# Performance work log

Measured on AMD Instinct MI355X. Metric: run time of the kernel, lower is better.

Reference implementation:

```python
import jax, jax.numpy as jnp
import numpy as np

MARGIN = 1.0
EPS = 1e-6  # torch.nn.PairwiseDistance default eps (added to the difference vector)


def setup_inputs() -> dict:
    key = jax.random.key(0)
    k1, k2 = jax.random.split(key)
    B, D = 8192, 256
    out = jax.random.normal(k1, (B, D), dtype=jnp.float32)
    label = jax.random.randint(k2, (B,), 0, 2, dtype=jnp.int64)
    return {"out": out, "label": label}


def reference(out, label):
    B, D = out.shape
    # PairwiseDistance: dist_ij = || out_i - out_j + eps ||_2
    # Expand: sum_k (d_k + eps)^2 = ||d||^2 + 2*eps*sum_k d_k + D*eps^2
    sq_norm = jnp.sum(out * out, axis=-1)                       # [B]
    gram = out @ out.T                                          # [B, B]
    sq = sq_norm[:, None] + sq_norm[None, :] - 2.0 * gram       # ||out_i - out_j||^2
    row_sum = jnp.sum(out, axis=-1)                             # [B]
    sq_eps = sq + 2.0 * EPS * (row_sum[:, None] - row_sum[None, :]) + D * EPS * EPS
    dist = jnp.sqrt(jnp.maximum(sq_eps, 1e-12))                 # [B, B]

    same = label[:, None] == label[None, :]                     # [B, B] bool
    pos = dist * dist
    neg = jnp.square(jnp.maximum(MARGIN - dist, 0.0))
    per_pair = jnp.where(same, pos, neg)

    # only i < j pairs (strict upper triangle)
    tri = jnp.triu(jnp.ones((B, B), dtype=out.dtype), k=1)
    loss = jnp.sum(per_pair * tri)
    cnt = B * (B - 1) // 2
    return loss / (cnt + 1e-6)
```

## Files before the change

### kernel.cpp

```cpp
#include <hip/hip_runtime.h>
#include <hip/hip_bf16.h>
#include <hip/hip_fp8.h>

#define B_ 8192
#define D_ 256
#define EPS_ 1e-6f
#define MARGIN_ 1.0f
#define NT_ 64
#define NTILES_ (NT_ * (NT_ + 1) / 2)
#define CEPS_ ((float)D_ * EPS_ * EPS_)

typedef float floatx4 __attribute__((ext_vector_type(4)));

typedef __attribute__((address_space(3))) unsigned int lds_uint_t;
typedef __attribute__((address_space(1))) const unsigned int g_uint_t;

__device__ __forceinline__ void g2l16(const unsigned char* g, unsigned char* l) {
    __builtin_amdgcn_global_load_lds((g_uint_t*)g, (lds_uint_t*)l, 16, 0, 0);
}

#define XBF_BYTES (B_ * D_ * 2)
#define OFF_P      0
#define OFF_Q      8192
#define OFF_TP0    16384
#define OFF_TP1    81920
#define OFF_PPP    147456
#define OFF_QQP    147968
#define OFF_CP     148480
#define OFF_PMINP  148736
#define OFF_QMINP  148992
#define OFF_ACC    149248

__device__ __forceinline__ int trif(int t) { return (t * (129 - t)) / 2; }
__device__ __forceinline__ int decode_ti(int t) {
    int ti = (int)((129.0f - sqrtf(fmaxf(16641.0f - 8.0f * (float)t, 0.0f))) * 0.5f);
    ti = max(0, min(63, ti));
    while (trif(ti + 1) <= t) ++ti;
    while (trif(ti) > t) --ti;
    return ti;
}

__global__ __launch_bounds__(256) void prep_kernel(
    const float* __restrict__ x, const int* __restrict__ label,
    unsigned char* __restrict__ xq, float* __restrict__ fws) {
    float* p = fws + OFF_P;   float* q = fws + OFF_Q;
    float* Tp0 = fws + OFF_TP0; float* Tp1 = fws + OFF_TP1;
    float* PpP = fws + OFF_PPP; float* QqP = fws + OFF_QQP;
    float* CpP = fws + OFF_CP;
    float* pminP = fws + OFF_PMINP; float* qminP = fws + OFF_QMINP;
    float* acc = fws + OFF_ACC;

    __shared__ int lab_s[32];
    __shared__ float spl[32], sql[32];
    __shared__ float colbuf0[4][256], colbuf1[4][256];

    const int blk = blockIdx.x;
    const int r0 = blk * 32;
    const int tid = threadIdx.x, w = tid >> 6, lane = tid & 63;

    if (tid < 32) lab_s[tid] = label[r0 + tid];
    __syncthreads();

    floatx4 t0 = (floatx4)0.0f, t1 = (floatx4)0.0f;
    #pragma unroll
    for (int i = 0; i < 8; ++i) {
        const int rloc = w * 8 + i;
        const int row = r0 + rloc;
        const floatx4 v = *(const floatx4*)(x + (size_t)row * D_ + lane * 4);
        float sq = v[0]*v[0] + v[1]*v[1] + v[2]*v[2] + v[3]*v[3];
        float rs = v[0] + v[1] + v[2] + v[3];
        #pragma unroll
        for (int off = 32; off; off >>= 1) {
            sq += __shfl_down(sq, off);
            rs += __shfl_down(rs, off);
        }
        if (lane == 0) {
            const float pv = sq + 2.0f * EPS_ * rs;
            const float qv = sq - 2.0f * EPS_ * rs;
            p[row] = pv; q[row] = qv; spl[rloc] = pv; sql[rloc] = qv;
        }
        if (lab_s[rloc]) t1 += v; else t0 += v;
        __hip_fp8_e4m3 c0(v[0]), c1(v[1]), c2(v[2]), c3(v[3]);
        const unsigned int u = (unsigned int)c0.__x | ((unsigned int)c1.__x << 8)
                             | ((unsigned int)c2.__x << 16) | ((unsigned int)c3.__x << 24);
        *(unsigned int*)(xq + (size_t)row * D_ + lane * 4) = u;
    }
    *(floatx4*)&colbuf0[w][lane * 4] = t0;
    *(floatx4*)&colbuf1[w][lane * 4] = t1;
    __syncthreads();

    {
        const int c = tid;
        Tp0[blk * 256 + c] = colbuf0[0][c] + colbuf0[1][c] + colbuf0[2][c] + colbuf0[3][c];
        Tp1[blk * 256 + c] = colbuf1[0][c] + colbuf1[1][c] + colbuf1[2][c] + colbuf1[3][c];
    }
    if (tid < 64) {
        const bool va = tid < 32;
        const float pv = va ? spl[tid & 31] : 0.0f;
        const float qv = va ? sql[tid & 31] : 0.0f;
        const int lb = va ? lab_s[tid & 31] : 0;
        float p0 = (va && !lb) ? pv : 0.0f, p1 = (va && lb) ? pv : 0.0f;
        float q0 = (va && !lb) ? qv : 0.0f, q1 = (va && lb) ? qv : 0.0f;
        float c0 = (va && !lb) ? 1.0f : 0.0f;
        float pm = va ? pv : 1e30f, qm = va ? qv : 1e30f;
        #pragma unroll
        for (int off = 32; off; off >>= 1) {
            p0 += __shfl_down(p0, off); p1 += __shfl_down(p1, off);
            q0 += __shfl_down(q0, off); q1 += __shfl_down(q1, off);
            c0 += __shfl_down(c0, off);
            pm = fminf(pm, __shfl_down(pm, off));
            qm = fminf(qm, __shfl_down(qm, off));
        }
        if (tid == 0) {
            PpP[blk * 2 + 0] = p0; PpP[blk * 2 + 1] = p1;
            QqP[blk * 2 + 0] = q0; QqP[blk * 2 + 1] = q1;
            CpP[blk] = c0; pminP[blk] = pm; qminP[blk] = qm;
            if (blk == 0) acc[0] = 0.0f;
        }
    }
}

__global__ __launch_bounds__(256, 2) void tile_kernel(
    const unsigned char* __restrict__ xq, const float* __restrict__ x,
    const int* __restrict__ label, const float* __restrict__ fws,
    float* __restrict__ acc) {
    const float* p = fws + OFF_P;  const float* q = fws + OFF_Q;
    const float* pminP = fws + OFF_PMINP; const float* qminP = fws + OFF_QMINP;

    const int ti = decode_ti(blockIdx.x);
    const int tj = ti + (blockIdx.x - trif(ti));
    const int i0 = ti * 128, j0 = tj * 128;

    __shared__ __align__(16) unsigned char As[128 * 256];
    __shared__ __align__(16) unsigned char Bs[128 * 256];

    const int tid = threadIdx.x, wave = tid >> 6, lane = tid & 63;
    const int quad = lane >> 4, r = lane & 15;
    const int wm = wave >> 1, wn = wave & 1;

    const int rL4 = lane >> 4, c16 = lane & 15;
    {
        const unsigned char* gA = xq + (size_t)(i0 + wave * 32) * D_;
        const unsigned char* gB = xq + (size_t)(j0 + wave * 32) * D_;
        #pragma unroll
        for (int i = 0; i < 8; ++i) {
            const int rr = i * 4 + rL4;
            const int key = rr & 7;
            const int srcoff = rr * 256 + ((c16 ^ key) * 16);
            g2l16(gA + srcoff, &As[(wave * 32 + i * 4) * 256]);
            g2l16(gB + srcoff, &Bs[(wave * 32 + i * 4) * 256]);
        }
    }

    int rbA[4], rbB[4];
    #pragma unroll
    for (int mt = 0; mt < 4; ++mt) rbA[mt] = (wm * 64 + mt * 16 + r) * 256;
    #pragma unroll
    for (int nt = 0; nt < 4; ++nt) rbB[nt] = (wn * 64 + nt * 16 + r) * 256;
    const int q8 = (quad & 1) * 8, qh = quad >> 1, r7 = r & 7;

    floatx4 accv[16];
    #pragma unroll
    for (int t = 0; t < 16; ++t) accv[t] = (floatx4)0.0f;

    __syncthreads();

    #pragma unroll
    for (int kb = 0; kb < 8; ++kb) {
        const int pcb = (((kb * 2 + qh) ^ r7) * 16) + q8;
        long av[4], bv[4];
        #pragma unroll
        for (int mt = 0; mt < 4; ++mt) av[mt] = *(const long*)(As + rbA[mt] + pcb);
        #pragma unroll
        for (int nt = 0; nt < 4; ++nt) bv[nt] = *(const long*)(Bs + rbB[nt] + pcb);
        #pragma unroll
        for (int mt = 0; mt < 4; ++mt)
            #pragma unroll
            for (int nt = 0; nt < 4; ++nt)
                accv[mt * 4 + nt] = __builtin_amdgcn_mfma_f32_16x16x32_fp8_fp8(
                    av[mt], bv[nt], accv[mt * 4 + nt], 0, 0, 0);
    }

    if (ti != tj) {
        float m = -1e30f;
        #pragma unroll
        for (int t = 0; t < 16; ++t)
            m = fmaxf(m, fmaxf(fmaxf(accv[t][0], accv[t][1]), fmaxf(accv[t][2], accv[t][3])));
        const float pmn = fminf(fminf(pminP[4 * ti], pminP[4 * ti + 1]),
                                fminf(pminP[4 * ti + 2], pminP[4 * ti + 3]));
        const float qmn = fminf(fminf(qminP[4 * tj], qminP[4 * tj + 1]),
                                fminf(qminP[4 * tj + 2], qminP[4 * tj + 3]));
        const float thr = (pmn + qmn + CEPS_ - 1.0f) * 0.5f - 16.0f;
        if (__any(m > thr)) {
            float s = 0.0f;
            #pragma unroll
            for (int mt = 0; mt < 4; ++mt)
                #pragma unroll
                for (int nt = 0; nt < 4; ++nt)
                    #pragma unroll
                    for (int reg = 0; reg < 4; ++reg) {
                        const int gi = i0 + wm * 64 + mt * 16 + quad * 4 + reg;
                        const int gj = j0 + wn * 64 + nt * 16 + r;
                        const float sq8 = p[gi] + q[gj] + CEPS_ - 2.0f * accv[mt * 4 + nt][reg];
                        if (sq8 < 33.0f && label[gi] != label[gj]) {
                            const float* xi = x + (size_t)gi * D_;
                            const float* xj = x + (size_t)gj * D_;
                            float sq = 0.0f;
                            for (int k = 0; k < D_; ++k) {
                                const float df = xi[k] - xj[k] + EPS_;
                                sq += df * df;
                            }
                            if (sq < 1.0f) {
                                const float d = sqrtf(fmaxf(sq, 1e-12f));
                                const float h = MARGIN_ - d;
                                s += h * h;
                            }
                        }
                    }
            #pragma unroll
            for (int off = 32; off; off >>= 1) s += __shfl_down(s, off);
            if (lane == 0) atomicAdd(acc, s);
        }
    } else {
        float s = 0.0f;
        #pragma unroll
        for (int mt = 0; mt < 4; ++mt)
            #pragma unroll
            for (int nt = 0; nt < 4; ++nt)
                #pragma unroll
                for (int reg = 0; reg < 4; ++reg) {
                    const int il = wm * 64 + mt * 16 + quad * 4 + reg;
                    const int jl = wn * 64 + nt * 16 + r;
                    if (il < jl) {
                        const int gi = i0 + il, gj = j0 + jl;
                        const float sq = p[gi] + q[gj] + CEPS_ - 2.0f * accv[mt * 4 + nt][reg];
                        const float d = sqrtf(fmaxf(sq, 1e-12f));
                        float v;
                        if (label[gi] == label[gj]) v = d * d;
                        else { const float h = fmaxf(MARGIN_ - d, 0.0f); v = h * h; }
                        s += v;
                    }
                }
        #pragma unroll
        for (int off = 32; off; off >>= 1) s += __shfl_down(s, off);
        if (lane == 0) atomicAdd(acc, s);
    }
}

__global__ __launch_bounds__(256) void finalize_kernel(
    const float* __restrict__ fws, float* __restrict__ out) {
    const float* Tp0 = fws + OFF_TP0; const float* Tp1 = fws + OFF_TP1;
    const float* PpP = fws + OFF_PPP; const float* QqP = fws + OFF_QQP;
    const float* CpP = fws + OFF_CP;
    const float* acc = fws + OFF_ACC;

    __shared__ floatx4 s0q[4][64], s1q[4][64], ssq[4][64];
    __shared__ float g2s;
    __shared__ double tP0[64], tP1[64], tQ0[64], tQ1[64], tC0[64];

    const int tid = threadIdx.x;
    const int quad = tid & 63, tq = tid >> 6;

    floatx4 a0 = (floatx4)0.0f, a1 = (floatx4)0.0f, as = (floatx4)0.0f;
    for (int t = tq; t < 64; t += 4) {
        floatx4 T0 = (floatx4)0.0f, T1 = (floatx4)0.0f;
        #pragma unroll
        for (int b4 = 0; b4 < 4; ++b4) {
            const int blk = 4 * t + b4;
            T0 += *(const floatx4*)&Tp0[blk * 256 + quad * 4];
            T1 += *(const floatx4*)&Tp1[blk * 256 + quad * 4];
        }
        a0 += T0; as += T0 * T0;
        a1 += T1; as += T1 * T1;
    }
    s0q[tq][quad] = a0; s1q[tq][quad] = a1; ssq[tq][quad] = as;

    if (tid >= 64 && tid < 128) {
        const int t = tid - 64;
        double P0 = 0, P1 = 0, Q0 = 0, Q1 = 0, C0 = 0;
        #pragma unroll
        for (int b4 = 0; b4 < 4; ++b4) {
            const int blk = 4 * t + b4;
            P0 += PpP[blk * 2]; P1 += PpP[blk * 2 + 1];
            Q0 += QqP[blk * 2]; Q1 += QqP[blk * 2 + 1];
            C0 += CpP[blk];
        }
        tP0[t] = P0; tP1[t] = P1; tQ0[t] = Q0; tQ1[t] = Q1; tC0[t] = C0;
    }
    __syncthreads();

    if (tid < 64) {
        const floatx4 S0 = s0q[0][tid] + s0q[1][tid] + s0q[2][tid] + s0q[3][tid];
        const floatx4 S1 = s1q[0][tid] + s1q[1][tid] + s1q[2][tid] + s1q[3][tid];
        const floatx4 SS = ssq[0][tid] + ssq[1][tid] + ssq[2][tid] + ssq[3][tid];
        float c = S0[0]*S0[0] + S0[1]*S0[1] + S0[2]*S0[2] + S0[3]*S0[3]
                + S1[0]*S1[0] + S1[1]*S1[1] + S1[2]*S1[2] + S1[3]*S1[3]
                - (SS[0] + SS[1] + SS[2] + SS[3]);
        #pragma unroll
        for (int off = 32; off; off >>= 1) c += __shfl_down(c, off);
        if (tid == 0) g2s = c;
    }
    __syncthreads();

    if (tid == 0) {
        double cross = -(double)g2s;
        double sufC0 = 0, sufC1 = 0, sufQ0 = 0, sufQ1 = 0;
        for (int t = 63; t >= 0; --t) {
            const double C0 = tC0[t], C1 = 128.0 - C0;
            cross += tP0[t] * sufC0 + tP1[t] * sufC1 + sufQ0 * C0 + sufQ1 * C1
                   + (double)CEPS_ * (C0 * sufC0 + C1 * sufC1);
            sufC0 += C0; sufC1 += C1; sufQ0 += tQ0[t]; sufQ1 += tQ1[t];
        }
        const double total = cross + (double)acc[0];
        const double cnt = (double)B_ * (double)(B_ - 1) / 2.0 + 1e-6;
        out[0] = (float)(total / cnt);
    }
}

extern "C" void kernel_launch(void* const* d_in, const int* in_sizes, int n_in,
                              void* d_out, int out_size, void* d_ws, size_t ws_size,
                              hipStream_t stream) {
    const float* x = (const float*)d_in[0];
    const int* label = (const int*)d_in[1];
    float* out = (float*)d_out;

    char* ws = (char*)d_ws;
    unsigned char* xq = (unsigned char*)ws;
    float* fws = (float*)(ws + XBF_BYTES);
    float* acc = fws + OFF_ACC;

    prep_kernel<<<B_ / 32, 256, 0, stream>>>(x, label, xq, fws);
    tile_kernel<<<NTILES_, 256, 0, stream>>>(xq, x, label, fws, acc);
    finalize_kernel<<<1, 256, 0, stream>>>(fws, out);
}
```

Measured before the change: 105.2 us.

## Fuse finalize into tile kernel, use 16x16x128 scaled FP8 MFMA with split-K LDS

Removes the separate finalize launch: the last tile block, found with an atomic completion counter, performs the final reduction. The GEMM now loads K in two 128-byte halves into a smaller LDS buffer and issues the wider mfma_scale 16x16x128 FP8 instruction instead of 16x16x32. Launch bounds are raised to 3 blocks per SM for occupancy. The risks are an extra sync inside the K loop and a serial tail in the last block.

```diff
diff --git a/kernel.cpp b/kernel.cpp
--- a/kernel.cpp
+++ b/kernel.cpp
@@ -11,6 +11,8 @@
 #define CEPS_ ((float)D_ * EPS_ * EPS_)
 
 typedef float floatx4 __attribute__((ext_vector_type(4)));
+typedef int intx4 __attribute__((ext_vector_type(4)));
+typedef int intx8 __attribute__((ext_vector_type(8)));
 
 typedef __attribute__((address_space(3))) unsigned int lds_uint_t;
 typedef __attribute__((address_space(1))) const unsigned int g_uint_t;
@@ -30,6 +32,7 @@
 #define OFF_PMINP  148736
 #define OFF_QMINP  148992
 #define OFF_ACC    149248
+#define OFF_DONE   149250
 
 __device__ __forceinline__ int trif(int t) { return (t * (129 - t)) / 2; }
 __device__ __forceinline__ int decode_ti(int t) {
@@ -39,6 +42,12 @@
     while (trif(ti) > t) --ti;
     return ti;
 }
+
+struct FinalShared {
+    floatx4 s0q[4][64], s1q[4][64], ssq[4][64];
+    double tP0[64], tP1[64], tQ0[64], tQ1[64], tC0[64];
+    float g2s;
+};
 
 __global__ __launch_bounds__(256) void prep_kernel(
     const float* __restrict__ x, const int* __restrict__ label,
@@ -48,7 +57,6 @@
     float* PpP = fws + OFF_PPP; float* QqP = fws + OFF_QQP;
     float* CpP = fws + OFF_CP;
     float* pminP = fws + OFF_PMINP; float* qminP = fws + OFF_QMINP;
-    float* acc = fws + OFF_ACC;
 
     __shared__ int lab_s[32];
     __shared__ float spl[32], sql[32];
@@ -115,70 +123,81 @@
             PpP[blk * 2 + 0] = p0; PpP[blk * 2 + 1] = p1;
             QqP[blk * 2 + 0] = q0; QqP[blk * 2 + 1] = q1;
             CpP[blk] = c0; pminP[blk] = pm; qminP[blk] = qm;
-            if (blk == 0) acc[0] = 0.0f;
-        }
-    }
-}
-
-__global__ __launch_bounds__(256, 2) void tile_kernel(
+            if (blk == 0) {
+                fws[OFF_ACC] = 0.0f;
+                ((unsigned*)(fws + OFF_DONE))[0] = 0u;
+            }
+        }
+    }
+}
+
+__global__ __launch_bounds__(256, 3) void tile_kernel(
     const unsigned char* __restrict__ xq, const float* __restrict__ x,
-    const int* __restrict__ label, const float* __restrict__ fws,
-    float* __restrict__ acc) {
+    const int* __restrict__ label, float* __restrict__ fws,
+    float* __restrict__ out) {
     const float* p = fws + OFF_P;  const float* q = fws + OFF_Q;
     const float* pminP = fws + OFF_PMINP; const float* qminP = fws + OFF_QMINP;
+    float* acc = fws + OFF_ACC;
+    unsigned* done = (unsigned*)(fws + OFF_DONE);
 
     const int ti = decode_ti(blockIdx.x);
     const int tj = ti + (blockIdx.x - trif(ti));
     const int i0 = ti * 128, j0 = tj * 128;
 
-    __shared__ __align__(16) unsigned char As[128 * 256];
-    __shared__ __align__(16) unsigned char Bs[128 * 256];
+    __shared__ union {
+        struct { __align__(16) unsigned char A[128 * 128], B[128 * 128]; } m;
+        FinalShared f;
+    } sh;
+    __shared__ int last_s;
 
     const int tid = threadIdx.x, wave = tid >> 6, lane = tid & 63;
-    const int quad = lane >> 4, r = lane & 15;
+    const int quad = lane >> 4, r = lane & 15, r7 = r & 7;
     const int wm = wave >> 1, wn = wave & 1;
 
-    const int rL4 = lane >> 4, c16 = lane & 15;
-    {
-        const unsigned char* gA = xq + (size_t)(i0 + wave * 32) * D_;
-        const unsigned char* gB = xq + (size_t)(j0 + wave * 32) * D_;
-        #pragma unroll
-        for (int i = 0; i < 8; ++i) {
-            const int rr = i * 4 + rL4;
-            const int key = rr & 7;
-            const int srcoff = rr * 256 + ((c16 ^ key) * 16);
-            g2l16(gA + srcoff, &As[(wave * 32 + i * 4) * 256]);
-            g2l16(gB + srcoff, &Bs[(wave * 32 + i * 4) * 256]);
-        }
-    }
+    const int rL8 = lane >> 3, cL = lane & 7;
+    const size_t lane_src = (size_t)rL8 * D_ + (size_t)((cL ^ rL8) * 16);
+    const unsigned char* gA0 = xq + (size_t)(i0 + wave * 32) * D_ + lane_src;
+    const unsigned char* gB0 = xq + (size_t)(j0 + wave * 32) * D_ + lane_src;
 
     int rbA[4], rbB[4];
     #pragma unroll
-    for (int mt = 0; mt < 4; ++mt) rbA[mt] = (wm * 64 + mt * 16 + r) * 256;
-    #pragma unroll
-    for (int nt = 0; nt < 4; ++nt) rbB[nt] = (wn * 64 + nt * 16 + r) * 256;
-    const int q8 = (quad & 1) * 8, qh = quad >> 1, r7 = r & 7;
+    for (int mt = 0; mt < 4; ++mt) rbA[mt] = (wm * 64 + mt * 16 + r) * 128;
+    #pragma unroll
+    for (int nt = 0; nt < 4; ++nt) rbB[nt] = (wn * 64 + nt * 16 + r) * 128;
+    const int co0 = ((2 * quad) ^ r7) * 16;
+    const int co1 = ((2 * quad + 1) ^ r7) * 16;
 
     floatx4 accv[16];
     #pragma unroll
     for (int t = 0; t < 16; ++t) accv[t] = (floatx4)0.0f;
 
-    __syncthreads();
-
-    #pragma unroll
-    for (int kb = 0; kb < 8; ++kb) {
-        const int pcb = (((kb * 2 + qh) ^ r7) * 16) + q8;
-        long av[4], bv[4];
-        #pragma unroll
-        for (int mt = 0; mt < 4; ++mt) av[mt] = *(const long*)(As + rbA[mt] + pcb);
-        #pragma unroll
-        for (int nt = 0; nt < 4; ++nt) bv[nt] = *(const long*)(Bs + rbB[nt] + pcb);
-        #pragma unroll
-        for (int mt = 0; mt < 4; ++mt)
+    #pragma unroll
+    for (int kh = 0; kh < 2; ++kh) {
+        if (kh) __syncthreads();
+        #pragma unroll
+        for (int i = 0; i < 4; ++i) {
+            g2l16(gA0 + (size_t)i * 8 * D_ + kh * 128, &sh.m.A[(wave * 32 + i * 8) * 128]);
+            g2l16(gB0 + (size_t)i * 8 * D_ + kh * 128, &sh.m.B[(wave * 32 + i * 8) * 128]);
+        }
+        __syncthreads();
+
+        intx8 bfr[4];
+        #pragma unroll
+        for (int nt = 0; nt < 4; ++nt) {
+            const intx4 lo = *(const intx4*)&sh.m.B[rbB[nt] + co0];
+            const intx4 hi = *(const intx4*)&sh.m.B[rbB[nt] + co1];
+            bfr[nt] = __builtin_shufflevector(lo, hi, 0, 1, 2, 3, 4, 5, 6, 7);
+        }
+        #pragma unroll
+        for (int mt = 0; mt < 4; ++mt) {
+            const intx4 lo = *(const intx4*)&sh.m.A[rbA[mt] + co0];
+            const intx4 hi = *(const intx4*)&sh.m.A[rbA[mt] + co1];
+            const intx8 af = __builtin_shufflevector(lo, hi, 0, 1, 2, 3, 4, 5, 6, 7);
             #pragma unroll
             for (int nt = 0; nt < 4; ++nt)
-                accv[mt * 4 + nt] = __builtin_amdgcn_mfma_f32_16x16x32_fp8_fp8(
-                    av[mt], bv[nt], accv[mt * 4 + nt], 0, 0, 0);
+                accv[mt * 4 + nt] = __builtin_amdgcn_mfma_scale_f32_16x16x128_f8f6f4(
+                    af, bfr[nt], accv[mt * 4 + nt], 0, 0, 0, 0x7F, 0, 0x7F);
+        }
     }
 
     if (ti != tj) {
@@ -245,75 +264,76 @@
         for (int off = 32; off; off >>= 1) s += __shfl_down(s, off);
         if (lane == 0) atomicAdd(acc, s);
     }
-}
-
-__global__ __launch_bounds__(256) void finalize_kernel(
-    const float* __restrict__ fws, float* __restrict__ out) {
-    const float* Tp0 = fws + OFF_TP0; const float* Tp1 = fws + OFF_TP1;
-    const float* PpP = fws + OFF_PPP; const float* QqP = fws + OFF_QQP;
-    const float* CpP = fws + OFF_CP;
-    const float* acc = fws + OFF_ACC;
-
-    __shared__ floatx4 s0q[4][64], s1q[4][64], ssq[4][64];
-    __shared__ float g2s;
-    __shared__ double tP0[64], tP1[64], tQ0[64], tQ1[64], tC0[64];
-
-    const int tid = threadIdx.x;
-    const int quad = tid & 63, tq = tid >> 6;
-
-    floatx4 a0 = (floatx4)0.0f, a1 = (floatx4)0.0f, as = (floatx4)0.0f;
-    for (int t = tq; t < 64; t += 4) {
-        floatx4 T0 = (floatx4)0.0f, T1 = (floatx4)0.0f;
-        #pragma unroll
-        for (int b4 = 0; b4 < 4; ++b4) {
-            const int blk = 4 * t + b4;
-            T0 += *(const floatx4*)&Tp0[blk * 256 + quad * 4];
-            T1 += *(const floatx4*)&Tp1[blk * 256 + quad * 4];
-        }
-        a0 += T0; as += T0 * T0;
-        a1 += T1; as += T1 * T1;
-    }
-    s0q[tq][quad] = a0; s1q[tq][quad] = a1; ssq[tq][quad] = as;
-
-    if (tid >= 64 && tid < 128) {
-        const int t = tid - 64;
-        double P0 = 0, P1 = 0, Q0 = 0, Q1 = 0, C0 = 0;
-        #pragma unroll
-        for (int b4 = 0; b4 < 4; ++b4) {
-            const int blk = 4 * t + b4;
-            P0 += PpP[blk * 2]; P1 += PpP[blk * 2 + 1];
-            Q0 += QqP[blk * 2]; Q1 += QqP[blk * 2 + 1];
-            C0 += CpP[blk];
-        }
-        tP0[t] = P0; tP1[t] = P1; tQ0[t] = Q0; tQ1[t] = Q1; tC0[t] = C0;
-    }
+
     __syncthreads();
-
-    if (tid < 64) {
-        const floatx4 S0 = s0q[0][tid] + s0q[1][tid] + s0q[2][tid] + s0q[3][tid];
-        const floatx4 S1 = s1q[0][tid] + s1q[1][tid] + s1q[2][tid] + s1q[3][tid];
-        const floatx4 SS = ssq[0][tid] + ssq[1][tid] + ssq[2][tid] + ssq[3][tid];
-        float c = S0[0]*S0[0] + S0[1]*S0[1] + S0[2]*S0[2] + S0[3]*S0[3]
-                + S1[0]*S1[0] + S1[1]*S1[1] + S1[2]*S1[2] + S1[3]*S1[3]
-                - (SS[0] + SS[1] + SS[2] + SS[3]);
-        #pragma unroll
-        for (int off = 32; off; off >>= 1) c += __shfl_down(c, off);
-        if (tid == 0) g2s = c;
+    if (tid == 0) {
+        __threadfence();
+        last_s = (atomicAdd(done, 1u) == NTILES_ - 1u);
     }
     __syncthreads();
-
-    if (tid == 0) {
-        double cross = -(double)g2s;
-        double sufC0 = 0, sufC1 = 0, sufQ0 = 0, sufQ1 = 0;
-        for (int t = 63; t >= 0; --t) {
-            const double C0 = tC0[t], C1 = 128.0 - C0;
-            cross += tP0[t] * sufC0 + tP1[t] * sufC1 + sufQ0 * C0 + sufQ1 * C1
-                   + (double)CEPS_ * (C0 * sufC0 + C1 * sufC1);
-            sufC0 += C0; sufC1 += C1; sufQ0 += tQ0[t]; sufQ1 += tQ1[t];
-        }
-        const double total = cross + (double)acc[0];
-        const double cnt = (double)B_ * (double)(B_ - 1) / 2.0 + 1e-6;
-        out[0] = (float)(total / cnt);
+    if (!last_s) return;
+
+    {
+        const float* Tp0 = fws + OFF_TP0; const float* Tp1 = fws + OFF_TP1;
+        const float* PpP = fws + OFF_PPP; const float* QqP = fws + OFF_QQP;
+        const float* CpP = fws + OFF_CP;
+        FinalShared& F = sh.f;
+        const int quad64 = tid & 63, tq = tid >> 6;
+
+        floatx4 a0 = (floatx4)0.0f, a1 = (floatx4)0.0f, as = (floatx4)0.0f;
+        for (int t = tq; t < 64; t += 4) {
+            floatx4 T0 = (floatx4)0.0f, T1 = (floatx4)0.0f;
+            #pragma unroll
+            for (int b4 = 0; b4 < 4; ++b4) {
+                const int blk = 4 * t + b4;
+                T0 += *(const floatx4*)&Tp0[blk * 256 + quad64 * 4];
+                T1 += *(const floatx4*)&Tp1[blk * 256 + quad64 * 4];
+            }
+            a0 += T0; as += T0 * T0;
+            a1 += T1; as += T1 * T1;
+        }
+        F.s0q[tq][quad64] = a0; F.s1q[tq][quad64] = a1; F.ssq[tq][quad64] = as;
+
+        if (tid >= 64 && tid < 128) {
+            const int t = tid - 64;
+            double P0 = 0, P1 = 0, Q0 = 0, Q1 = 0, C0 = 0;
+            #pragma unroll
+            for (int b4 = 0; b4 < 4; ++b4) {
+                const int blk = 4 * t + b4;
+                P0 += PpP[blk * 2]; P1 += PpP[blk * 2 + 1];
+                Q0 += QqP[blk * 2]; Q1 += QqP[blk * 2 + 1];
+                C0 += CpP[blk];
+            }
+            F.tP0[t] = P0; F.tP1[t] = P1; F.tQ0[t] = Q0; F.tQ1[t] = Q1; F.tC0[t] = C0;
+        }
+        __syncthreads();
+
+        if (tid < 64) {
+            const floatx4 S0 = F.s0q[0][tid] + F.s0q[1][tid] + F.s0q[2][tid] + F.s0q[3][tid];
+            const floatx4 S1 = F.s1q[0][tid] + F.s1q[1][tid] + F.s1q[2][tid] + F.s1q[3][tid];
+            const floatx4 SS = F.ssq[0][tid] + F.ssq[1][tid] + F.ssq[2][tid] + F.ssq[3][tid];
+            float c = S0[0]*S0[0] + S0[1]*S0[1] + S0[2]*S0[2] + S0[3]*S0[3]
+                    + S1[0]*S1[0] + S1[1]*S1[1] + S1[2]*S1[2] + S1[3]*S1[3]
+                    - (SS[0] + SS[1] + SS[2] + SS[3]);
+            #pragma unroll
+            for (int off = 32; off; off >>= 1) c += __shfl_down(c, off);
+            if (tid == 0) F.g2s = c;
+        }
+        __syncthreads();
+
+        if (tid == 0) {
+            double cross = -(double)F.g2s;
+            double sufC0 = 0, sufC1 = 0, sufQ0 = 0, sufQ1 = 0;
+            for (int t = 63; t >= 0; --t) {
+                const double C0 = F.tC0[t], C1 = 128.0 - C0;
+                cross += F.tP0[t] * sufC0 + F.tP1[t] * sufC1 + sufQ0 * C0 + sufQ1 * C1
+                       + (double)CEPS_ * (C0 * sufC0 + C1 * sufC1);
+                sufC0 += C0; sufC1 += C1; sufQ0 += F.tQ0[t]; sufQ1 += F.tQ1[t];
+            }
+            const double total = cross + (double)atomicAdd(acc, 0.0f);
+            const double cnt = (double)B_ * (double)(B_ - 1) / 2.0 + 1e-6;
+            out[0] = (float)(total / cnt);
+        }
     }
 }
 
@@ -327,9 +347,7 @@
     char* ws = (char*)d_ws;
     unsigned char* xq = (unsigned char*)ws;
     float* fws = (float*)(ws + XBF_BYTES);
-    float* acc = fws + OFF_ACC;
 
     prep_kernel<<<B_ / 32, 256, 0, stream>>>(x, label, xq, fws);
-    tile_kernel<<<NTILES_, 256, 0, stream>>>(xq, x, label, fws, acc);
-    finalize_kernel<<<1, 256, 0, stream>>>(fws, out);
-}
+    tile_kernel<<<NTILES_, 256, 0, stream>>>(xq, x, label, fws, out);
+}
```

After: 129.1 us. +22.7%, slower.

## Split pair tiles into 128x64 blocks of 8 waves with block-level reduction

Applied to the files above, without the earlier changes.

The triangular tile grid changes from 128x128 tiles with 4 waves to 128x64 tiles with 8 waves. That doubles the block count, and each wave now computes a 32x32 sub-tile with far fewer accumulator registers. The aim is better occupancy, better load balance across CUs, and more latency hiding for the FP8 MFMA work and the sparse exact-distance refinement. Per-wave partial sums are now combined in LDS, and each block issues one atomic, skipped when the sum is zero and the tile does not overlap the diagonal. The cost is that the A tile is reloaded twice as often, and the tile-index decode has to handle a new row/column mapping.

```diff
diff --git a/kernel.cpp b/kernel.cpp
--- a/kernel.cpp
+++ b/kernel.cpp
@@ -7,7 +7,8 @@
 #define EPS_ 1e-6f
 #define MARGIN_ 1.0f
 #define NT_ 64
-#define NTILES_ (NT_ * (NT_ + 1) / 2)
+#define NJT_ 128
+#define NBLK_ 4160
 #define CEPS_ ((float)D_ * EPS_ * EPS_)
 
 typedef float floatx4 __attribute__((ext_vector_type(4)));
@@ -31,14 +32,7 @@
 #define OFF_QMINP  148992
 #define OFF_ACC    149248
 
-__device__ __forceinline__ int trif(int t) { return (t * (129 - t)) / 2; }
-__device__ __forceinline__ int decode_ti(int t) {
-    int ti = (int)((129.0f - sqrtf(fmaxf(16641.0f - 8.0f * (float)t, 0.0f))) * 0.5f);
-    ti = max(0, min(63, ti));
-    while (trif(ti + 1) <= t) ++ti;
-    while (trif(ti) > t) --ti;
-    return ti;
-}
+__device__ __forceinline__ int cumf(int t) { return t * (129 - t); }
 
 __global__ __launch_bounds__(256) void prep_kernel(
     const float* __restrict__ x, const int* __restrict__ label,
@@ -48,7 +42,6 @@
     float* PpP = fws + OFF_PPP; float* QqP = fws + OFF_QQP;
     float* CpP = fws + OFF_CP;
     float* pminP = fws + OFF_PMINP; float* qminP = fws + OFF_QMINP;
-    float* acc = fws + OFF_ACC;
 
     __shared__ int lab_s[32];
     __shared__ float spl[32], sql[32];
@@ -115,93 +108,100 @@
             PpP[blk * 2 + 0] = p0; PpP[blk * 2 + 1] = p1;
             QqP[blk * 2 + 0] = q0; QqP[blk * 2 + 1] = q1;
             CpP[blk] = c0; pminP[blk] = pm; qminP[blk] = qm;
-            if (blk == 0) acc[0] = 0.0f;
-        }
-    }
-}
-
-__global__ __launch_bounds__(256, 2) void tile_kernel(
+            if (blk == 0) fws[OFF_ACC] = 0.0f;
+        }
+    }
+}
+
+__global__ __launch_bounds__(512, 6) void tile_kernel(
     const unsigned char* __restrict__ xq, const float* __restrict__ x,
     const int* __restrict__ label, const float* __restrict__ fws,
     float* __restrict__ acc) {
     const float* p = fws + OFF_P;  const float* q = fws + OFF_Q;
     const float* pminP = fws + OFF_PMINP; const float* qminP = fws + OFF_QMINP;
 
-    const int ti = decode_ti(blockIdx.x);
-    const int tj = ti + (blockIdx.x - trif(ti));
-    const int i0 = ti * 128, j0 = tj * 128;
+    const int b = blockIdx.x;
+    int ti = (int)((129.0f - sqrtf((float)(16641 - 4 * b))) * 0.5f);
+    ti = max(0, min(63, ti));
+    while (cumf(ti + 1) <= b) ++ti;
+    while (cumf(ti) > b) --ti;
+    const int jj = 2 * ti + (b - cumf(ti));
+    const int i0 = ti * 128, j0 = jj * 64;
+    const bool overlap = (j0 < i0 + 128);
 
     __shared__ __align__(16) unsigned char As[128 * 256];
-    __shared__ __align__(16) unsigned char Bs[128 * 256];
+    __shared__ __align__(16) unsigned char Bs[64 * 256];
+    __shared__ float wsum[8];
 
     const int tid = threadIdx.x, wave = tid >> 6, lane = tid & 63;
-    const int quad = lane >> 4, r = lane & 15;
+    const int quad = lane >> 4, r = lane & 15, r7 = r & 7;
     const int wm = wave >> 1, wn = wave & 1;
 
     const int rL4 = lane >> 4, c16 = lane & 15;
     {
-        const unsigned char* gA = xq + (size_t)(i0 + wave * 32) * D_;
-        const unsigned char* gB = xq + (size_t)(j0 + wave * 32) * D_;
-        #pragma unroll
-        for (int i = 0; i < 8; ++i) {
-            const int rr = i * 4 + rL4;
-            const int key = rr & 7;
-            const int srcoff = rr * 256 + ((c16 ^ key) * 16);
-            g2l16(gA + srcoff, &As[(wave * 32 + i * 4) * 256]);
-            g2l16(gB + srcoff, &Bs[(wave * 32 + i * 4) * 256]);
-        }
-    }
-
-    int rbA[4], rbB[4];
-    #pragma unroll
-    for (int mt = 0; mt < 4; ++mt) rbA[mt] = (wm * 64 + mt * 16 + r) * 256;
-    #pragma unroll
-    for (int nt = 0; nt < 4; ++nt) rbB[nt] = (wn * 64 + nt * 16 + r) * 256;
-    const int q8 = (quad & 1) * 8, qh = quad >> 1, r7 = r & 7;
-
-    floatx4 accv[16];
-    #pragma unroll
-    for (int t = 0; t < 16; ++t) accv[t] = (floatx4)0.0f;
+        #pragma unroll
+        for (int i = 0; i < 4; ++i) {
+            const int row = wave * 16 + i * 4 + rL4;
+            const int src = row * 256 + ((c16 ^ (row & 7)) * 16);
+            g2l16(xq + (size_t)i0 * 256 + src, &As[(wave * 16 + i * 4) * 256]);
+        }
+        #pragma unroll
+        for (int i = 0; i < 2; ++i) {
+            const int row = wave * 8 + i * 4 + rL4;
+            const int src = row * 256 + ((c16 ^ (row & 7)) * 16);
+            g2l16(xq + (size_t)j0 * 256 + src, &Bs[(wave * 8 + i * 4) * 256]);
+        }
+    }
+
+    int rbA[2], rbB[2];
+    #pragma unroll
+    for (int mt = 0; mt < 2; ++mt) rbA[mt] = (wm * 32 + mt * 16 + r) * 256;
+    #pragma unroll
+    for (int nt = 0; nt < 2; ++nt) rbB[nt] = (wn * 32 + nt * 16 + r) * 256;
+    const int q8 = (quad & 1) * 8, qh = quad >> 1;
+
+    floatx4 accv[4];
+    #pragma unroll
+    for (int t = 0; t < 4; ++t) accv[t] = (floatx4)0.0f;
 
     __syncthreads();
 
     #pragma unroll
     for (int kb = 0; kb < 8; ++kb) {
         const int pcb = (((kb * 2 + qh) ^ r7) * 16) + q8;
-        long av[4], bv[4];
-        #pragma unroll
-        for (int mt = 0; mt < 4; ++mt) av[mt] = *(const long*)(As + rbA[mt] + pcb);
-        #pragma unroll
-        for (int nt = 0; nt < 4; ++nt) bv[nt] = *(const long*)(Bs + rbB[nt] + pcb);
-        #pragma unroll
-        for (int mt = 0; mt < 4; ++mt)
+        long av[2], bv[2];
+        #pragma unroll
+        for (int mt = 0; mt < 2; ++mt) av[mt] = *(const long*)(As + rbA[mt] + pcb);
+        #pragma unroll
+        for (int nt = 0; nt < 2; ++nt) bv[nt] = *(const long*)(Bs + rbB[nt] + pcb);
+        #pragma unroll
+        for (int mt = 0; mt < 2; ++mt)
             #pragma unroll
-            for (int nt = 0; nt < 4; ++nt)
-                accv[mt * 4 + nt] = __builtin_amdgcn_mfma_f32_16x16x32_fp8_fp8(
-                    av[mt], bv[nt], accv[mt * 4 + nt], 0, 0, 0);
-    }
-
-    if (ti != tj) {
+            for (int nt = 0; nt < 2; ++nt)
+                accv[mt * 2 + nt] = __builtin_amdgcn_mfma_f32_16x16x32_fp8_fp8(
+                    av[mt], bv[nt], accv[mt * 2 + nt], 0, 0, 0);
+    }
+
+    float s = 0.0f;
+    if (!overlap) {
         float m = -1e30f;
         #pragma unroll
-        for (int t = 0; t < 16; ++t)
+        for (int t = 0; t < 4; ++t)
             m = fmaxf(m, fmaxf(fmaxf(accv[t][0], accv[t][1]), fmaxf(accv[t][2], accv[t][3])));
         const float pmn = fminf(fminf(pminP[4 * ti], pminP[4 * ti + 1]),
                                 fminf(pminP[4 * ti + 2], pminP[4 * ti + 3]));
-        const float qmn = fminf(fminf(qminP[4 * tj], qminP[4 * tj + 1]),
-                                fminf(qminP[4 * tj + 2], qminP[4 * tj + 3]));
+        const float qmn = fminf(qminP[2 * jj], qminP[2 * jj + 1]);
         const float thr = (pmn + qmn + CEPS_ - 1.0f) * 0.5f - 16.0f;
         if (__any(m > thr)) {
-            float s = 0.0f;
             #pragma unroll
-            for (int mt = 0; mt < 4; ++mt)
+            for (int mt = 0; mt < 2; ++mt)
                 #pragma unroll
-                for (int nt = 0; nt < 4; ++nt)
+                for (int nt = 0; nt < 2; ++nt)
                     #pragma unroll
                     for (int reg = 0; reg < 4; ++reg) {
-                        const int gi = i0 + wm * 64 + mt * 16 + quad * 4 + reg;
-                        const int gj = j0 + wn * 64 + nt * 16 + r;
-                        const float sq8 = p[gi] + q[gj] + CEPS_ - 2.0f * accv[mt * 4 + nt][reg];
+                        const int gi = i0 + wm * 32 + mt * 16 + quad * 4 + reg;
+                        const int gj = j0 + wn * 32 + nt * 16 + r;
+                        const float sq8 = p[gi] + q[gj] + CEPS_ - 2.0f * accv[mt * 2 + nt][reg];
                         if (sq8 < 33.0f && label[gi] != label[gj]) {
                             const float* xi = x + (size_t)gi * D_;
                             const float* xj = x + (size_t)gj * D_;
@@ -217,23 +217,18 @@
                             }
                         }
                     }
+        }
+    } else {
+        #pragma unroll
+        for (int mt = 0; mt < 2; ++mt)
             #pragma unroll
-            for (int off = 32; off; off >>= 1) s += __shfl_down(s, off);
-            if (lane == 0) atomicAdd(acc, s);
-        }
-    } else {
-        float s = 0.0f;
-        #pragma unroll
-        for (int mt = 0; mt < 4; ++mt)
-            #pragma unroll
-            for (int nt = 0; nt < 4; ++nt)
+            for (int nt = 0; nt < 2; ++nt)
                 #pragma unroll
                 for (int reg = 0; reg < 4; ++reg) {
-                    const int il = wm * 64 + mt * 16 + quad * 4 + reg;
-                    const int jl = wn * 64 + nt * 16 + r;
-                    if (il < jl) {
-                        const int gi = i0 + il, gj = j0 + jl;
-                        const float sq = p[gi] + q[gj] + CEPS_ - 2.0f * accv[mt * 4 + nt][reg];
+                    const int gi = i0 + wm * 32 + mt * 16 + quad * 4 + reg;
+                    const int gj = j0 + wn * 32 + nt * 16 + r;
+                    if (gi < gj) {
+                        const float sq = p[gi] + q[gj] + CEPS_ - 2.0f * accv[mt * 2 + nt][reg];
                         const float d = sqrtf(fmaxf(sq, 1e-12f));
                         float v;
                         if (label[gi] == label[gj]) v = d * d;
@@ -241,9 +236,15 @@
                         s += v;
                     }
                 }
-        #pragma unroll
-        for (int off = 32; off; off >>= 1) s += __shfl_down(s, off);
-        if (lane == 0) atomicAdd(acc, s);
+    }
+    #pragma unroll
+    for (int off = 32; off; off >>= 1) s += __shfl_down(s, off);
+    if (lane == 0) wsum[wave] = s;
+    __syncthreads();
+    if (tid == 0) {
+        const float t = (wsum[0] + wsum[1]) + (wsum[2] + wsum[3])
+                      + (wsum[4] + wsum[5]) + (wsum[6] + wsum[7]);
+        if (t != 0.0f || overlap) atomicAdd(acc, t);
     }
 }
 
@@ -330,6 +331,6 @@
     float* acc = fws + OFF_ACC;
 
     prep_kernel<<<B_ / 32, 256, 0, stream>>>(x, label, xq, fws);
-    tile_kernel<<<NTILES_, 256, 0, stream>>>(xq, x, label, fws, acc);
+    tile_kernel<<<NBLK_, 512, 0, stream>>>(xq, x, label, fws, acc);
     finalize_kernel<<<1, 256, 0, stream>>>(fws, out);
 }
```

Result: no change. 105.3 us (+0.0%).

## Screen pairs with a 64-dim fp8 partial Gram and compute same-label loss in closed form

Applied to the files above, without the earlier changes.

The tile kernel now builds an fp8 Gram over only the first 64 feature dimensions and reads the operands straight from global memory into registers, with no LDS staging. A partial squared distance is a lower bound on the full one, so pairs whose partial distance clears a threshold are skipped, and the rest fall back to an exact fp32 hinge. The same-label (positive) term is computed for all pairs in closed form in finalize from per-class norms and column sums, so diagonal tiles no longer evaluate it per pair. This cuts per-tile load and MFMA work by about four times. In exchange, correctness depends on the fixed screen margin covering the fp8 quantisation error.

```diff
diff --git a/kernel.cpp b/kernel.cpp
--- a/kernel.cpp
+++ b/kernel.cpp
@@ -4,20 +4,15 @@
 
 #define B_ 8192
 #define D_ 256
+#define KS_ 64
 #define EPS_ 1e-6f
 #define MARGIN_ 1.0f
 #define NT_ 64
 #define NTILES_ (NT_ * (NT_ + 1) / 2)
 #define CEPS_ ((float)D_ * EPS_ * EPS_)
+#define SCREEN_ 17.0f
 
 typedef float floatx4 __attribute__((ext_vector_type(4)));
-
-typedef __attribute__((address_space(3))) unsigned int lds_uint_t;
-typedef __attribute__((address_space(1))) const unsigned int g_uint_t;
-
-__device__ __forceinline__ void g2l16(const unsigned char* g, unsigned char* l) {
-    __builtin_amdgcn_global_load_lds((g_uint_t*)g, (lds_uint_t*)l, 16, 0, 0);
-}
 
 #define XBF_BYTES (B_ * D_ * 2)
 #define OFF_P      0
@@ -40,18 +35,35 @@
     return ti;
 }
 
+__device__ __noinline__ float exact_hinge(const float* __restrict__ x, int gi, int gj,
+                                          const int* __restrict__ label) {
+    if (label[gi] == label[gj]) return 0.0f;
+    const float* xi = x + (size_t)gi * D_;
+    const float* xj = x + (size_t)gj * D_;
+    float sq = 0.0f;
+    for (int k = 0; k < D_; ++k) {
+        const float df = xi[k] - xj[k] + EPS_;
+        sq += df * df;
+    }
+    if (sq < 1.0f) {
+        const float d = sqrtf(fmaxf(sq, 1e-12f));
+        const float h = MARGIN_ - d;
+        return h * h;
+    }
+    return 0.0f;
+}
+
 __global__ __launch_bounds__(256) void prep_kernel(
     const float* __restrict__ x, const int* __restrict__ label,
-    unsigned char* __restrict__ xq, float* __restrict__ fws) {
-    float* p = fws + OFF_P;   float* q = fws + OFF_Q;
+    unsigned char* __restrict__ xqS, float* __restrict__ fws) {
+    float* pS = fws + OFF_P;   float* qS = fws + OFF_Q;
     float* Tp0 = fws + OFF_TP0; float* Tp1 = fws + OFF_TP1;
     float* PpP = fws + OFF_PPP; float* QqP = fws + OFF_QQP;
     float* CpP = fws + OFF_CP;
     float* pminP = fws + OFF_PMINP; float* qminP = fws + OFF_QMINP;
-    float* acc = fws + OFF_ACC;
 
     __shared__ int lab_s[32];
-    __shared__ float spl[32], sql[32];
+    __shared__ float spl[32], sql[32], spS[32], sqSl[32];
     __shared__ float colbuf0[4][256], colbuf1[4][256];
 
     const int blk = blockIdx.x;
@@ -61,6 +73,7 @@
     if (tid < 32) lab_s[tid] = label[r0 + tid];
     __syncthreads();
 
+    const float msk = (lane < 16) ? 1.0f : 0.0f;
     floatx4 t0 = (floatx4)0.0f, t1 = (floatx4)0.0f;
     #pragma unroll
     for (int i = 0; i < 8; ++i) {
@@ -69,21 +82,29 @@
         const floatx4 v = *(const floatx4*)(x + (size_t)row * D_ + lane * 4);
         float sq = v[0]*v[0] + v[1]*v[1] + v[2]*v[2] + v[3]*v[3];
         float rs = v[0] + v[1] + v[2] + v[3];
+        float sqP = msk * sq, rsP = msk * rs;
         #pragma unroll
         for (int off = 32; off; off >>= 1) {
-            sq += __shfl_down(sq, off);
-            rs += __shfl_down(rs, off);
+            sq  += __shfl_down(sq,  off);
+            rs  += __shfl_down(rs,  off);
+            sqP += __shfl_down(sqP, off);
+            rsP += __shfl_down(rsP, off);
         }
         if (lane == 0) {
-            const float pv = sq + 2.0f * EPS_ * rs;
-            const float qv = sq - 2.0f * EPS_ * rs;
-            p[row] = pv; q[row] = qv; spl[rloc] = pv; sql[rloc] = qv;
+            spl[rloc]  = sq + 2.0f * EPS_ * rs;
+            sql[rloc]  = sq - 2.0f * EPS_ * rs;
+            const float pSv = sqP + 2.0f * EPS_ * rsP;
+            const float qSv = sqP - 2.0f * EPS_ * rsP;
+            pS[row] = pSv; qS[row] = qSv;
+            spS[rloc] = pSv; sqSl[rloc] = qSv;
         }
         if (lab_s[rloc]) t1 += v; else t0 += v;
-        __hip_fp8_e4m3 c0(v[0]), c1(v[1]), c2(v[2]), c3(v[3]);
-        const unsigned int u = (unsigned int)c0.__x | ((unsigned int)c1.__x << 8)
-                             | ((unsigned int)c2.__x << 16) | ((unsigned int)c3.__x << 24);
-        *(unsigned int*)(xq + (size_t)row * D_ + lane * 4) = u;
+        if (lane < 16) {
+            __hip_fp8_e4m3 c0(v[0]), c1(v[1]), c2(v[2]), c3(v[3]);
+            const unsigned int u = (unsigned int)c0.__x | ((unsigned int)c1.__x << 8)
+                                 | ((unsigned int)c2.__x << 16) | ((unsigned int)c3.__x << 24);
+            *(unsigned int*)(xqS + (size_t)row * KS_ + lane * 4) = u;
+        }
     }
     *(floatx4*)&colbuf0[w][lane * 4] = t0;
     *(floatx4*)&colbuf1[w][lane * 4] = t1;
@@ -102,7 +123,8 @@
         float p0 = (va && !lb) ? pv : 0.0f, p1 = (va && lb) ? pv : 0.0f;
         float q0 = (va && !lb) ? qv : 0.0f, q1 = (va && lb) ? qv : 0.0f;
         float c0 = (va && !lb) ? 1.0f : 0.0f;
-        float pm = va ? pv : 1e30f, qm = va ? qv : 1e30f;
+        float pm = va ? spS[tid & 31] : 1e30f;
+        float qm = va ? sqSl[tid & 31] : 1e30f;
         #pragma unroll
         for (int off = 32; off; off >>= 1) {
             p0 += __shfl_down(p0, off); p1 += __shfl_down(p1, off);
@@ -115,72 +137,51 @@
             PpP[blk * 2 + 0] = p0; PpP[blk * 2 + 1] = p1;
             QqP[blk * 2 + 0] = q0; QqP[blk * 2 + 1] = q1;
             CpP[blk] = c0; pminP[blk] = pm; qminP[blk] = qm;
-            if (blk == 0) acc[0] = 0.0f;
-        }
-    }
-}
-
-__global__ __launch_bounds__(256, 2) void tile_kernel(
-    const unsigned char* __restrict__ xq, const float* __restrict__ x,
+            if (blk == 0) fws[OFF_ACC] = 0.0f;
+        }
+    }
+}
+
+__global__ __launch_bounds__(256, 3) void detect_kernel(
+    const unsigned char* __restrict__ xqS, const float* __restrict__ x,
     const int* __restrict__ label, const float* __restrict__ fws,
     float* __restrict__ acc) {
-    const float* p = fws + OFF_P;  const float* q = fws + OFF_Q;
+    const float* pS = fws + OFF_P;  const float* qS = fws + OFF_Q;
     const float* pminP = fws + OFF_PMINP; const float* qminP = fws + OFF_QMINP;
 
     const int ti = decode_ti(blockIdx.x);
     const int tj = ti + (blockIdx.x - trif(ti));
     const int i0 = ti * 128, j0 = tj * 128;
 
-    __shared__ __align__(16) unsigned char As[128 * 256];
-    __shared__ __align__(16) unsigned char Bs[128 * 256];
-
     const int tid = threadIdx.x, wave = tid >> 6, lane = tid & 63;
     const int quad = lane >> 4, r = lane & 15;
     const int wm = wave >> 1, wn = wave & 1;
 
-    const int rL4 = lane >> 4, c16 = lane & 15;
-    {
-        const unsigned char* gA = xq + (size_t)(i0 + wave * 32) * D_;
-        const unsigned char* gB = xq + (size_t)(j0 + wave * 32) * D_;
-        #pragma unroll
-        for (int i = 0; i < 8; ++i) {
-            const int rr = i * 4 + rL4;
-            const int key = rr & 7;
-            const int srcoff = rr * 256 + ((c16 ^ key) * 16);
-            g2l16(gA + srcoff, &As[(wave * 32 + i * 4) * 256]);
-            g2l16(gB + srcoff, &Bs[(wave * 32 + i * 4) * 256]);
-        }
-    }
-
-    int rbA[4], rbB[4];
-    #pragma unroll
-    for (int mt = 0; mt < 4; ++mt) rbA[mt] = (wm * 64 + mt * 16 + r) * 256;
-    #pragma unroll
-    for (int nt = 0; nt < 4; ++nt) rbB[nt] = (wn * 64 + nt * 16 + r) * 256;
-    const int q8 = (quad & 1) * 8, qh = quad >> 1, r7 = r & 7;
+    long av[8], bv[8];
+    #pragma unroll
+    for (int mt = 0; mt < 4; ++mt)
+        #pragma unroll
+        for (int ks = 0; ks < 2; ++ks) {
+            av[mt * 2 + ks] = *(const long*)(xqS +
+                (size_t)(i0 + wm * 64 + mt * 16 + r) * KS_ + ks * 32 + quad * 8);
+            bv[mt * 2 + ks] = *(const long*)(xqS +
+                (size_t)(j0 + wn * 64 + mt * 16 + r) * KS_ + ks * 32 + quad * 8);
+        }
 
     floatx4 accv[16];
     #pragma unroll
     for (int t = 0; t < 16; ++t) accv[t] = (floatx4)0.0f;
 
-    __syncthreads();
-
-    #pragma unroll
-    for (int kb = 0; kb < 8; ++kb) {
-        const int pcb = (((kb * 2 + qh) ^ r7) * 16) + q8;
-        long av[4], bv[4];
-        #pragma unroll
-        for (int mt = 0; mt < 4; ++mt) av[mt] = *(const long*)(As + rbA[mt] + pcb);
-        #pragma unroll
-        for (int nt = 0; nt < 4; ++nt) bv[nt] = *(const long*)(Bs + rbB[nt] + pcb);
+    #pragma unroll
+    for (int ks = 0; ks < 2; ++ks)
         #pragma unroll
         for (int mt = 0; mt < 4; ++mt)
             #pragma unroll
             for (int nt = 0; nt < 4; ++nt)
                 accv[mt * 4 + nt] = __builtin_amdgcn_mfma_f32_16x16x32_fp8_fp8(
-                    av[mt], bv[nt], accv[mt * 4 + nt], 0, 0, 0);
-    }
-
+                    av[mt * 2 + ks], bv[nt * 2 + ks], accv[mt * 4 + nt], 0, 0, 0);
+
+    float s = 0.0f;
     if (ti != tj) {
         float m = -1e30f;
         #pragma unroll
@@ -190,9 +191,7 @@
                                 fminf(pminP[4 * ti + 2], pminP[4 * ti + 3]));
         const float qmn = fminf(fminf(qminP[4 * tj], qminP[4 * tj + 1]),
                                 fminf(qminP[4 * tj + 2], qminP[4 * tj + 3]));
-        const float thr = (pmn + qmn + CEPS_ - 1.0f) * 0.5f - 16.0f;
-        if (__any(m > thr)) {
-            float s = 0.0f;
+        if (__any(2.0f * m > pmn + qmn - SCREEN_)) {
             #pragma unroll
             for (int mt = 0; mt < 4; ++mt)
                 #pragma unroll
@@ -201,28 +200,11 @@
                     for (int reg = 0; reg < 4; ++reg) {
                         const int gi = i0 + wm * 64 + mt * 16 + quad * 4 + reg;
                         const int gj = j0 + wn * 64 + nt * 16 + r;
-                        const float sq8 = p[gi] + q[gj] + CEPS_ - 2.0f * accv[mt * 4 + nt][reg];
-                        if (sq8 < 33.0f && label[gi] != label[gj]) {
-                            const float* xi = x + (size_t)gi * D_;
-                            const float* xj = x + (size_t)gj * D_;
-                            float sq = 0.0f;
-                            for (int k = 0; k < D_; ++k) {
-                                const float df = xi[k] - xj[k] + EPS_;
-                                sq += df * df;
-                            }
-                            if (sq < 1.0f) {
-                                const float d = sqrtf(fmaxf(sq, 1e-12f));
-                                const float h = MARGIN_ - d;
-                                s += h * h;
-                            }
-                        }
+                        const float sq8 = pS[gi] + qS[gj] - 2.0f * accv[mt * 4 + nt][reg];
+                        if (sq8 < SCREEN_) s += exact_hinge(x, gi, gj, label);
                     }
-            #pragma unroll
-            for (int off = 32; off; off >>= 1) s += __shfl_down(s, off);
-            if (lane == 0) atomicAdd(acc, s);
         }
     } else {
-        float s = 0.0f;
         #pragma unroll
         for (int mt = 0; mt < 4; ++mt)
             #pragma unroll
@@ -233,18 +215,14 @@
                     const int jl = wn * 64 + nt * 16 + r;
                     if (il < jl) {
                         const int gi = i0 + il, gj = j0 + jl;
-                        const float sq = p[gi] + q[gj] + CEPS_ - 2.0f * accv[mt * 4 + nt][reg];
-                        const float d = sqrtf(fmaxf(sq, 1e-12f));
-                        float v;
-                        if (label[gi] == label[gj]) v = d * d;
-                        else { const float h = fmaxf(MARGIN_ - d, 0.0f); v = h * h; }
-                        s += v;
+                        const float sq8 = pS[gi] + qS[gj] - 2.0f * accv[mt * 4 + nt][reg];
+                        if (sq8 < SCREEN_) s += exact_hinge(x, gi, gj, label);
                     }
                 }
-        #pragma unroll
-        for (int off = 32; off; off >>= 1) s += __shfl_down(s, off);
-        if (lane == 0) atomicAdd(acc, s);
-    }
+    }
+    #pragma unroll
+    for (int off = 32; off; off >>= 1) s += __shfl_down(s, off);
+    if (lane == 0 && s != 0.0f) atomicAdd(acc, s);
 }
 
 __global__ __launch_bounds__(256) void finalize_kernel(
@@ -254,64 +232,43 @@
     const float* CpP = fws + OFF_CP;
     const float* acc = fws + OFF_ACC;
 
-    __shared__ floatx4 s0q[4][64], s1q[4][64], ssq[4][64];
-    __shared__ float g2s;
-    __shared__ double tP0[64], tP1[64], tQ0[64], tQ1[64], tC0[64];
-
+    __shared__ float buf[256];
+    __shared__ double res[6];
     const int tid = threadIdx.x;
-    const int quad = tid & 63, tq = tid >> 6;
-
-    floatx4 a0 = (floatx4)0.0f, a1 = (floatx4)0.0f, as = (floatx4)0.0f;
-    for (int t = tq; t < 64; t += 4) {
-        floatx4 T0 = (floatx4)0.0f, T1 = (floatx4)0.0f;
-        #pragma unroll
-        for (int b4 = 0; b4 < 4; ++b4) {
-            const int blk = 4 * t + b4;
-            T0 += *(const floatx4*)&Tp0[blk * 256 + quad * 4];
-            T1 += *(const floatx4*)&Tp1[blk * 256 + quad * 4];
-        }
-        a0 += T0; as += T0 * T0;
-        a1 += T1; as += T1 * T1;
-    }
-    s0q[tq][quad] = a0; s1q[tq][quad] = a1; ssq[tq][quad] = as;
-
-    if (tid >= 64 && tid < 128) {
-        const int t = tid - 64;
-        double P0 = 0, P1 = 0, Q0 = 0, Q1 = 0, C0 = 0;
-        #pragma unroll
-        for (int b4 = 0; b4 < 4; ++b4) {
-            const int blk = 4 * t + b4;
-            P0 += PpP[blk * 2]; P1 += PpP[blk * 2 + 1];
-            Q0 += QqP[blk * 2]; Q1 += QqP[blk * 2 + 1];
-            C0 += CpP[blk];
-        }
-        tP0[t] = P0; tP1[t] = P1; tQ0[t] = Q0; tQ1[t] = Q1; tC0[t] = C0;
+
+    float S0 = 0.0f, S1 = 0.0f;
+    for (int b = 0; b < 256; ++b) {
+        S0 += Tp0[b * 256 + tid];
+        S1 += Tp1[b * 256 + tid];
+    }
+    float vals[6];
+    vals[0] = S0 * S0 + S1 * S1;
+    vals[1] = PpP[2 * tid]; vals[2] = PpP[2 * tid + 1];
+    vals[3] = QqP[2 * tid]; vals[4] = QqP[2 * tid + 1];
+    vals[5] = CpP[tid];
+
+    #pragma unroll
+    for (int vi = 0; vi < 6; ++vi) {
+        __syncthreads();
+        buf[tid] = vals[vi];
+        __syncthreads();
+        if (tid < 64) {
+            float a = buf[tid] + buf[tid + 64] + buf[tid + 128] + buf[tid + 192];
+            #pragma unroll
+            for (int off = 32; off; off >>= 1) a += __shfl_down(a, off);
+            if (tid == 0) res[vi] = (double)a;
+        }
     }
     __syncthreads();
 
-    if (tid < 64) {
-        const floatx4 S0 = s0q[0][tid] + s0q[1][tid] + s0q[2][tid] + s0q[3][tid];
-        const floatx4 S1 = s1q[0][tid] + s1q[1][tid] + s1q[2][tid] + s1q[3][tid];
-        const floatx4 SS = ssq[0][tid] + ssq[1][tid] + ssq[2][tid] + ssq[3][tid];
-        float c = S0[0]*S0[0] + S0[1]*S0[1] + S0[2]*S0[2] + S0[3]*S0[3]
-                + S1[0]*S1[0] + S1[1]*S1[1] + S1[2]*S1[2] + S1[3]*S1[3]
-                - (SS[0] + SS[1] + SS[2] + SS[3]);
-        #pragma unroll
-        for (int off = 32; off; off >>= 1) c += __shfl_down(c, off);
-        if (tid == 0) g2s = c;
-    }
-    __syncthreads();
-
     if (tid == 0) {
-        double cross = -(double)g2s;
-        double sufC0 = 0, sufC1 = 0, sufQ0 = 0, sufQ1 = 0;
-        for (int t = 63; t >= 0; --t) {
-            const double C0 = tC0[t], C1 = 128.0 - C0;
-            cross += tP0[t] * sufC0 + tP1[t] * sufC1 + sufQ0 * C0 + sufQ1 * C1
-                   + (double)CEPS_ * (C0 * sufC0 + C1 * sufC1);
-            sufC0 += C0; sufC1 += C1; sufQ0 += tQ0[t]; sufQ1 += tQ1[t];
-        }
-        const double total = cross + (double)acc[0];
+        const double Tsq = res[0];
+        const double P0 = res[1], P1 = res[2], Q0 = res[3], Q1 = res[4];
+        const double C0 = res[5], C1 = (double)B_ - C0;
+        const double same = 0.5 * (C0 * (P0 + Q0) + C1 * (P1 + Q1)
+                                 + (C0 * (C0 - 1.0) + C1 * (C1 - 1.0)) * (double)CEPS_
+                                 - 2.0 * Tsq);
+        const double total = same + (double)acc[0];
         const double cnt = (double)B_ * (double)(B_ - 1) / 2.0 + 1e-6;
         out[0] = (float)(total / cnt);
     }
@@ -325,11 +282,11 @@
     float* out = (float*)d_out;
 
     char* ws = (char*)d_ws;
-    unsigned char* xq = (unsigned char*)ws;
+    unsigned char* xqS = (unsigned char*)ws;
     float* fws = (float*)(ws + XBF_BYTES);
     float* acc = fws + OFF_ACC;
 
-    prep_kernel<<<B_ / 32, 256, 0, stream>>>(x, label, xq, fws);
-    tile_kernel<<<NTILES_, 256, 0, stream>>>(xq, x, label, fws, acc);
+    prep_kernel<<<B_ / 32, 256, 0, stream>>>(x, label, xqS, fws);
+    detect_kernel<<<NTILES_, 256, 0, stream>>>(xqS, x, label, fws, acc);
     finalize_kernel<<<1, 256, 0, stream>>>(fws, out);
 }
```

Result: faster. 98.65 us (-6.2%).
